# Kernel optimization log

Hardware: AMD Instinct MI355X
Metric: run time of the kernel (lower is better)

Reference implementation:

```python
import jax, jax.numpy as jnp
import numpy as np

B, S, E, H, U = 2048, 64, 512, 512, 512

def setup_inputs() -> dict:
    key = jax.random.key(0)
    ks = jax.random.split(key, 6)
    s = lambda d: 1.0 / np.sqrt(d)
    return {
        "features": jax.random.normal(ks[0], (B, S, E), jnp.float32),
        "hidden": jax.random.normal(ks[1], (B, H), jnp.float32),
        "W1": jax.random.normal(ks[2], (E, U), jnp.float32) * s(E),
        "b1": jnp.zeros((U,), jnp.float32),
        "W2": jax.random.normal(ks[3], (H, U), jnp.float32) * s(H),
        "b2": jnp.zeros((U,), jnp.float32),
        "Wv": jax.random.normal(ks[4], (U, 1), jnp.float32) * s(U),
        "bv": jnp.zeros((1,), jnp.float32),
    }

def reference(features, hidden, W1, b1, W2, b2, Wv, bv):
    # Bahdanau additive attention (dropout at inference = identity).
    h1 = jnp.einsum('bse,eu->bsu', features, W1) + b1          # [B,S,U]
    h2 = hidden @ W2 + b2                                       # [B,U]
    scores = jnp.tanh(h1 + h2[:, None, :]) @ Wv + bv            # [B,S,1]
    weights = jax.nn.softmax(scores, axis=1)                    # softmax over seq
    context = jnp.sum(weights * features, axis=1)               # [B,E]
    return context
```

## Files before the change

kernel.cpp:

```cpp
#include <hip/hip_runtime.h>

typedef _Float16 f16x8 __attribute__((ext_vector_type(8)));
typedef unsigned short u16x4 __attribute__((ext_vector_type(4)));
typedef float f32x4 __attribute__((ext_vector_type(4)));

#define VMWAIT(N) asm volatile("s_waitcnt vmcnt(" #N ")" ::: "memory")

__global__ void convert_w_kernel(const float* __restrict__ w1,
                                 const float* __restrict__ w2,
                                 unsigned short* __restrict__ w1img,
                                 unsigned short* __restrict__ w2img) {
    int u = blockIdx.x;
    int k = threadIdx.x + blockIdx.y * 256;
    size_t idx = (size_t)(k >> 5) * 16384 + (size_t)u * 32 + (k & 31);
    _Float16 h1 = (_Float16)w1[(size_t)k * 512 + u];
    _Float16 h2 = (_Float16)w2[(size_t)k * 512 + u];
    w1img[idx] = __builtin_bit_cast(unsigned short, h1);
    w2img[idx] = __builtin_bit_cast(unsigned short, h2);
}

__device__ __forceinline__ void stage_a64(const float* __restrict__ src,
                                          char* As, int tid) {
    const int row = tid >> 2, q = tid & 3;
    const float* p = src + (size_t)row * 512 + q * 4;
    const int sw2 = ((row >> 1) & 3) << 4;
    char* wb = As + row * 64;
    float4 va[4], vb[4];
#define AISS(V, G) { _Pragma("unroll") \
    for (int j_ = 0; j_ < 4; ++j_) V[j_] = *(const float4*)(p + ((G) * 4 + j_) * 16); }
#define APRC(V, G) { _Pragma("unroll") \
    for (int j_ = 0; j_ < 4; ++j_) { \
        const int i_ = (G) * 4 + j_; \
        u16x4 h_; \
        h_[0] = __builtin_bit_cast(unsigned short, (_Float16)V[j_].x); \
        h_[1] = __builtin_bit_cast(unsigned short, (_Float16)V[j_].y); \
        h_[2] = __builtin_bit_cast(unsigned short, (_Float16)V[j_].z); \
        h_[3] = __builtin_bit_cast(unsigned short, (_Float16)V[j_].w); \
        *(u16x4*)(wb + (i_ >> 1) * 4096 + ((q * 8 + (i_ & 1) * 32) ^ sw2)) = h_; } }
    AISS(va, 0); AISS(vb, 1);
    VMWAIT(4); APRC(va, 0); AISS(va, 2);
    VMWAIT(4); APRC(vb, 1); AISS(vb, 3);
    VMWAIT(4); APRC(va, 2); AISS(va, 4);
    VMWAIT(4); APRC(vb, 3); AISS(vb, 5);
    VMWAIT(4); APRC(va, 4); AISS(va, 6);
    VMWAIT(4); APRC(vb, 5); AISS(vb, 7);
    VMWAIT(4); APRC(va, 6);
    VMWAIT(0); APRC(vb, 7);
#undef AISS
#undef APRC
}

__device__ __forceinline__ void chunk_gemm(const char* __restrict__ bcol,
                                           const char* As, const int* aoff,
                                           f32x4 acc[4][4]) {
    f16x8 brA[4], brB[4], afA[4], afB[4];
    #pragma unroll
    for (int i = 0; i < 4; ++i)
        #pragma unroll
        for (int j = 0; j < 4; ++j) acc[i][j] = (f32x4){0.f, 0.f, 0.f, 0.f};
    #pragma unroll
    for (int j = 0; j < 4; ++j) brA[j] = *(const f16x8*)(bcol + j * 1024);
    #pragma unroll
    for (int j = 0; j < 4; ++j) brB[j] = *(const f16x8*)(bcol + 32768 + j * 1024);
    #pragma unroll
    for (int i = 0; i < 4; ++i) afA[i] = *(const f16x8*)(As + aoff[i]);

    #pragma unroll
    for (int tt = 0; tt < 8; ++tt) {
        const int t0 = 2 * tt, t1 = t0 + 1;
        if (t0 < 15) {
            #pragma unroll
            for (int i = 0; i < 4; ++i)
                afB[i] = *(const f16x8*)(As + t1 * 4096 + aoff[i]);
        }
        VMWAIT(4);
        #pragma unroll
        for (int i = 0; i < 4; ++i)
            #pragma unroll
            for (int j = 0; j < 4; ++j)
                acc[i][j] = __builtin_amdgcn_mfma_f32_16x16x32_f16(afA[i], brA[j], acc[i][j], 0, 0, 0);
        if (t0 < 14) {
            #pragma unroll
            for (int j = 0; j < 4; ++j)
                brA[j] = *(const f16x8*)(bcol + (t0 + 2) * 32768 + j * 1024);
        }
        if (t1 < 15) {
            #pragma unroll
            for (int i = 0; i < 4; ++i)
                afA[i] = *(const f16x8*)(As + (t1 + 1) * 4096 + aoff[i]);
        }
        if (t1 < 14) { VMWAIT(4); } else { VMWAIT(0); }
        #pragma unroll
        for (int i = 0; i < 4; ++i)
            #pragma unroll
            for (int j = 0; j < 4; ++j)
                acc[i][j] = __builtin_amdgcn_mfma_f32_16x16x32_f16(afB[i], brB[j], acc[i][j], 0, 0, 0);
        if (t1 < 14) {
            #pragma unroll
            for (int j = 0; j < 4; ++j)
                brB[j] = *(const f16x8*)(bcol + (t1 + 2) * 32768 + j * 1024);
        }
    }
}

__global__ __launch_bounds__(256, 2)
void h2_gemm_kernel(const float* __restrict__ hidden,
                    const char* __restrict__ w2img,
                    const float* __restrict__ b2,
                    float* __restrict__ h2o) {
    __shared__ char As[65536];
    const int tid = threadIdx.x, bm = blockIdx.x;
    const int lane = tid & 63, wid = tid >> 6;
    const int lane16 = lane & 15, g = lane >> 4;
    stage_a64(hidden + (size_t)bm * 32768, As, tid);
    __syncthreads();
    const int swA = (lane16 >> 1) & 3;
    int aoff[4];
    #pragma unroll
    for (int i = 0; i < 4; ++i)
        aoff[i] = (i * 16 + lane16) * 64 + ((g ^ swA) << 4);
    #pragma unroll
    for (int c = 0; c < 2; ++c) {
        const char* bcol = w2img + (size_t)(wid * 128 + c * 64 + lane16) * 64 + g * 16;
        f32x4 acc[4][4];
        chunk_gemm(bcol, As, aoff, acc);
        #pragma unroll
        for (int j = 0; j < 4; ++j) {
            int col = wid * 128 + c * 64 + j * 16 + lane16;
            float bb = b2[col];
            #pragma unroll
            for (int i = 0; i < 4; ++i)
                #pragma unroll
                for (int r = 0; r < 4; ++r)
                    h2o[(size_t)(bm * 64 + i * 16 + g * 4 + r) * 512 + col] = acc[i][j][r] + bb;
        }
    }
}

__global__ __launch_bounds__(256, 2)
void fused_all_kernel(const float* __restrict__ feat,
                      const char* __restrict__ w1img,
                      const float* __restrict__ h2,
                      const float* __restrict__ b1,
                      const float* __restrict__ wv,
                      float* __restrict__ out) {
    __shared__ char As[65536];
    __shared__ float spl[256];
    __shared__ float wsm[64];
    const int tid = threadIdx.x, bm = blockIdx.x;
    const int lane = tid & 63, wid = tid >> 6;
    const int lane16 = lane & 15, g = lane >> 4;

    stage_a64(feat + (size_t)bm * 32768, As, tid);
    __syncthreads();

    float hhv[8], wvv[8];
    #pragma unroll
    for (int j = 0; j < 8; ++j) {
        int u = wid * 128 + j * 16 + lane16;
        hhv[j] = b1[u] + h2[(size_t)bm * 512 + u];
        wvv[j] = wv[u];
    }
    VMWAIT(0);

    const int swA = (lane16 >> 1) & 3;
    int aoff[4];
    #pragma unroll
    for (int i = 0; i < 4; ++i)
        aoff[i] = (i * 16 + lane16) * 64 + ((g ^ swA) << 4);

    float sacc[16];
    #pragma unroll
    for (int x = 0; x < 16; ++x) sacc[x] = 0.f;

    #pragma unroll
    for (int c = 0; c < 2; ++c) {
        const char* bcol = w1img + (size_t)(wid * 128 + c * 64 + lane16) * 64 + g * 16;
        f32x4 acc[4][4];
        chunk_gemm(bcol, As, aoff, acc);
        #pragma unroll
        for (int i = 0; i < 4; ++i)
            #pragma unroll
            for (int r = 0; r < 4; ++r) {
                float s = 0.f;
                #pragma unroll
                for (int j = 0; j < 4; ++j) {
                    float h = acc[i][j][r] + hhv[c * 4 + j];
                    float ex = __expf(2.f * h);
                    s += (1.f - 2.f * __builtin_amdgcn_rcpf(ex + 1.f)) * wvv[c * 4 + j];
                }
                sacc[i * 4 + r] += s;
            }
    }

    #pragma unroll
    for (int i = 0; i < 4; ++i)
        #pragma unroll
        for (int r = 0; r < 4; ++r) {
            float s = sacc[i * 4 + r];
            s += __shfl_xor(s, 1); s += __shfl_xor(s, 2);
            s += __shfl_xor(s, 4); s += __shfl_xor(s, 8);
            if (lane16 == 0) spl[(i * 16 + g * 4 + r) * 4 + wid] = s;
        }
    __syncthreads();

    if (tid < 64) {
        float s = (spl[tid * 4 + 0] + spl[tid * 4 + 1]) +
                  (spl[tid * 4 + 2] + spl[tid * 4 + 3]);
        float m = s;
        #pragma unroll
        for (int off = 32; off; off >>= 1) m = fmaxf(m, __shfl_xor(m, off));
        float e = __expf(s - m);
        float sum = e;
        #pragma unroll
        for (int off = 32; off; off >>= 1) sum += __shfl_xor(sum, off);
        wsm[tid] = e / sum;
    }
    __syncthreads();

    {
        const int cseg = (tid >> 4) * 4096;
        const int cin = (tid & 15) * 4;
        float ax = 0.f, ay = 0.f;
        #pragma unroll 8
        for (int s = 0; s < 64; ++s) {
            unsigned v = *(const unsigned*)(As + cseg + s * 64 +
                                            (cin ^ (((s >> 1) & 3) << 4)));
            float w = wsm[s];
            ax += w * (float)__builtin_bit_cast(_Float16, (unsigned short)(v & 0xffffu));
            ay += w * (float)__builtin_bit_cast(_Float16, (unsigned short)(v >> 16));
        }
        ((float2*)out)[(size_t)bm * 256 + tid] = make_float2(ax, ay);
    }
}

extern "C" void kernel_launch(void* const* d_in, const int* in_sizes, int n_in,
                              void* d_out, int out_size, void* d_ws, size_t ws_size,
                              hipStream_t stream) {
    (void)in_sizes; (void)n_in; (void)out_size; (void)ws_size;
    const float* feat   = (const float*)d_in[0];
    const float* hidden = (const float*)d_in[1];
    const float* W1     = (const float*)d_in[2];
    const float* b1     = (const float*)d_in[3];
    const float* W2     = (const float*)d_in[4];
    const float* b2     = (const float*)d_in[5];
    const float* Wv     = (const float*)d_in[6];
    float* out = (float*)d_out;

    char* ws = (char*)d_ws;
    unsigned short* w1img = (unsigned short*)(ws);
    unsigned short* w2img = (unsigned short*)(ws + 524288);
    float* h2 = (float*)(ws + 1048576);

    convert_w_kernel<<<dim3(512, 2), dim3(256), 0, stream>>>(W1, W2, w1img, w2img);
    h2_gemm_kernel<<<dim3(32), dim3(256), 0, stream>>>(hidden, (const char*)w2img, b2, h2);
    fused_all_kernel<<<dim3(2048), dim3(256), 0, stream>>>(feat, (const char*)w1img, h2, b1, Wv, out);
}
```

Baseline: 149.6 us.

## Warp-specialize fused attention kernel with producer waves double-buffering feature tiles

The fused kernel now handles four batch rows per 512-thread block. Four consumer waves run the GEMM, tanh-score, softmax and context steps, while four producer waves load and convert the next batch's features into a second 64KB LDS buffer. Each consumer wave now covers 128 output columns in a single pass using 4x8 MFMA tiles, with s_setprio raised around the MFMA bursts. The aim is to hide the global feature loads behind MFMA work. In exchange, the block needs 128KB+ of LDS (which may limit it to one block per CU), carries higher register pressure, and adds raw barriers.

New measurement: 580.3 us. +288.0%, slower.

```diff
diff --git a/kernel.cpp b/kernel.cpp
--- a/kernel.cpp
+++ b/kernel.cpp
@@ -5,6 +5,18 @@
 typedef float f32x4 __attribute__((ext_vector_type(4)));
 
 #define VMWAIT(N) asm volatile("s_waitcnt vmcnt(" #N ")" ::: "memory")
+#define LGKM0()   asm volatile("s_waitcnt lgkmcnt(0)" ::: "memory")
+#define RBAR()    do { asm volatile("" ::: "memory"); __builtin_amdgcn_s_barrier(); \
+                       asm volatile("" ::: "memory"); } while (0)
+
+__device__ __forceinline__ u16x4 cvt4(float4 v) {
+    u16x4 h;
+    h[0] = __builtin_bit_cast(unsigned short, (_Float16)v.x);
+    h[1] = __builtin_bit_cast(unsigned short, (_Float16)v.y);
+    h[2] = __builtin_bit_cast(unsigned short, (_Float16)v.z);
+    h[3] = __builtin_bit_cast(unsigned short, (_Float16)v.w);
+    return h;
+}
 
 __global__ void convert_w_kernel(const float* __restrict__ w1,
                                  const float* __restrict__ w2,
@@ -31,12 +43,7 @@
 #define APRC(V, G) { _Pragma("unroll") \
     for (int j_ = 0; j_ < 4; ++j_) { \
         const int i_ = (G) * 4 + j_; \
-        u16x4 h_; \
-        h_[0] = __builtin_bit_cast(unsigned short, (_Float16)V[j_].x); \
-        h_[1] = __builtin_bit_cast(unsigned short, (_Float16)V[j_].y); \
-        h_[2] = __builtin_bit_cast(unsigned short, (_Float16)V[j_].z); \
-        h_[3] = __builtin_bit_cast(unsigned short, (_Float16)V[j_].w); \
-        *(u16x4*)(wb + (i_ >> 1) * 4096 + ((q * 8 + (i_ & 1) * 32) ^ sw2)) = h_; } }
+        *(u16x4*)(wb + (i_ >> 1) * 4096 + ((q * 8 + (i_ & 1) * 32) ^ sw2)) = cvt4(V[j_]); } }
     AISS(va, 0); AISS(vb, 1);
     VMWAIT(4); APRC(va, 0); AISS(va, 2);
     VMWAIT(4); APRC(vb, 1); AISS(vb, 3);
@@ -64,15 +71,12 @@
     for (int j = 0; j < 4; ++j) brB[j] = *(const f16x8*)(bcol + 32768 + j * 1024);
     #pragma unroll
     for (int i = 0; i < 4; ++i) afA[i] = *(const f16x8*)(As + aoff[i]);
-
     #pragma unroll
     for (int tt = 0; tt < 8; ++tt) {
         const int t0 = 2 * tt, t1 = t0 + 1;
-        if (t0 < 15) {
-            #pragma unroll
-            for (int i = 0; i < 4; ++i)
-                afB[i] = *(const f16x8*)(As + t1 * 4096 + aoff[i]);
-        }
+        #pragma unroll
+        for (int i = 0; i < 4; ++i)
+            afB[i] = *(const f16x8*)(As + t1 * 4096 + aoff[i]);
         VMWAIT(4);
         #pragma unroll
         for (int i = 0; i < 4; ++i)
@@ -114,11 +118,10 @@
     const int lane16 = lane & 15, g = lane >> 4;
     stage_a64(hidden + (size_t)bm * 32768, As, tid);
     __syncthreads();
-    const int swA = (lane16 >> 1) & 3;
     int aoff[4];
     #pragma unroll
     for (int i = 0; i < 4; ++i)
-        aoff[i] = (i * 16 + lane16) * 64 + ((g ^ swA) << 4);
+        aoff[i] = (i * 16 + lane16) * 64 + ((g ^ ((lane16 >> 1) & 3)) << 4);
     #pragma unroll
     for (int c = 0; c < 2; ++c) {
         const char* bcol = w2img + (size_t)(wid * 128 + c * 64 + lane16) * 64 + g * 16;
@@ -137,100 +140,190 @@
     }
 }
 
-__global__ __launch_bounds__(256, 2)
+__device__ __forceinline__ void chunk128(const char* __restrict__ bcol,
+                                         const char* As, const int* aoff,
+                                         f32x4 acc[4][8]) {
+    f16x8 brA[8], brB[8], afA[4], afB[4];
+    #pragma unroll
+    for (int i = 0; i < 4; ++i)
+        #pragma unroll
+        for (int j = 0; j < 8; ++j) acc[i][j] = (f32x4){0.f, 0.f, 0.f, 0.f};
+    #pragma unroll
+    for (int j = 0; j < 8; ++j) brA[j] = *(const f16x8*)(bcol + j * 1024);
+    #pragma unroll
+    for (int j = 0; j < 8; ++j) brB[j] = *(const f16x8*)(bcol + 32768 + j * 1024);
+    #pragma unroll
+    for (int i = 0; i < 4; ++i) afA[i] = *(const f16x8*)(As + aoff[i]);
+    #pragma unroll
+    for (int tt = 0; tt < 8; ++tt) {
+        const int t0 = 2 * tt, t1 = t0 + 1;
+        #pragma unroll
+        for (int i = 0; i < 4; ++i)
+            afB[i] = *(const f16x8*)(As + t1 * 4096 + aoff[i]);
+        VMWAIT(8);
+        __builtin_amdgcn_s_setprio(1);
+        #pragma unroll
+        for (int i = 0; i < 4; ++i)
+            #pragma unroll
+            for (int j = 0; j < 8; ++j)
+                acc[i][j] = __builtin_amdgcn_mfma_f32_16x16x32_f16(afA[i], brA[j], acc[i][j], 0, 0, 0);
+        __builtin_amdgcn_s_setprio(0);
+        if (t0 < 14) {
+            #pragma unroll
+            for (int j = 0; j < 8; ++j)
+                brA[j] = *(const f16x8*)(bcol + (t0 + 2) * 32768 + j * 1024);
+        }
+        if (t1 < 15) {
+            #pragma unroll
+            for (int i = 0; i < 4; ++i)
+                afA[i] = *(const f16x8*)(As + (t1 + 1) * 4096 + aoff[i]);
+        }
+        if (t1 < 14) { VMWAIT(8); } else { VMWAIT(0); }
+        __builtin_amdgcn_s_setprio(1);
+        #pragma unroll
+        for (int i = 0; i < 4; ++i)
+            #pragma unroll
+            for (int j = 0; j < 8; ++j)
+                acc[i][j] = __builtin_amdgcn_mfma_f32_16x16x32_f16(afB[i], brB[j], acc[i][j], 0, 0, 0);
+        __builtin_amdgcn_s_setprio(0);
+        if (t1 < 14) {
+            #pragma unroll
+            for (int j = 0; j < 8; ++j)
+                brB[j] = *(const f16x8*)(bcol + (t1 + 2) * 32768 + j * 1024);
+        }
+    }
+}
+
+__global__ __launch_bounds__(512, 2)
 void fused_all_kernel(const float* __restrict__ feat,
                       const char* __restrict__ w1img,
                       const float* __restrict__ h2,
                       const float* __restrict__ b1,
                       const float* __restrict__ wv,
                       float* __restrict__ out) {
-    __shared__ char As[65536];
+    __shared__ char As[2][65536];
     __shared__ float spl[256];
     __shared__ float wsm[64];
-    const int tid = threadIdx.x, bm = blockIdx.x;
-    const int lane = tid & 63, wid = tid >> 6;
-    const int lane16 = lane & 15, g = lane >> 4;
-
-    stage_a64(feat + (size_t)bm * 32768, As, tid);
-    __syncthreads();
-
-    float hhv[8], wvv[8];
-    #pragma unroll
-    for (int j = 0; j < 8; ++j) {
-        int u = wid * 128 + j * 16 + lane16;
-        hhv[j] = b1[u] + h2[(size_t)bm * 512 + u];
-        wvv[j] = wv[u];
-    }
-    VMWAIT(0);
-
-    const int swA = (lane16 >> 1) & 3;
+
+    const int tid = threadIdx.x;
+    const int b0 = blockIdx.x * 4;
+    const bool consumer = (tid < 256);
+    const int lane16 = tid & 15, g = (tid >> 4) & 3;
+    const int wid = tid >> 6;
+
+    {
+        const int row = tid >> 3, q = tid & 7;
+        const float* p = feat + (size_t)b0 * 32768 + (size_t)row * 512 + q * 4;
+        char* wb = As[0] + row * 64 + ((q * 8) ^ (((row >> 1) & 3) << 4));
+        float4 v[16];
+        #pragma unroll
+        for (int i = 0; i < 16; ++i) v[i] = *(const float4*)(p + i * 32);
+        VMWAIT(12);
+        #pragma unroll
+        for (int i = 0; i < 4; ++i)   *(u16x4*)(wb + i * 4096) = cvt4(v[i]);
+        VMWAIT(8);
+        #pragma unroll
+        for (int i = 4; i < 8; ++i)   *(u16x4*)(wb + i * 4096) = cvt4(v[i]);
+        VMWAIT(4);
+        #pragma unroll
+        for (int i = 8; i < 12; ++i)  *(u16x4*)(wb + i * 4096) = cvt4(v[i]);
+        VMWAIT(0);
+        #pragma unroll
+        for (int i = 12; i < 16; ++i) *(u16x4*)(wb + i * 4096) = cvt4(v[i]);
+    }
+    LGKM0();
+    RBAR();
+
     int aoff[4];
     #pragma unroll
     for (int i = 0; i < 4; ++i)
-        aoff[i] = (i * 16 + lane16) * 64 + ((g ^ swA) << 4);
-
-    float sacc[16];
-    #pragma unroll
-    for (int x = 0; x < 16; ++x) sacc[x] = 0.f;
-
-    #pragma unroll
-    for (int c = 0; c < 2; ++c) {
-        const char* bcol = w1img + (size_t)(wid * 128 + c * 64 + lane16) * 64 + g * 16;
-        f32x4 acc[4][4];
-        chunk_gemm(bcol, As, aoff, acc);
-        #pragma unroll
-        for (int i = 0; i < 4; ++i)
-            #pragma unroll
-            for (int r = 0; r < 4; ++r) {
-                float s = 0.f;
+        aoff[i] = (i * 16 + lane16) * 64 + ((g ^ ((lane16 >> 1) & 3)) << 4);
+    const char* bcol = w1img + (size_t)(wid * 128 + lane16) * 64 + g * 16;
+
+    const int prow = (tid & 255) >> 2, pq = tid & 3;
+    const int psw2 = ((prow >> 1) & 3) << 4;
+
+    #pragma unroll 1
+    for (int it = 0; it < 4; ++it) {
+        const int cur = it & 1;
+        const int b = b0 + it;
+        float4 pv[16];
+        if (consumer) {
+            f32x4 acc[4][8];
+            chunk128(bcol, As[cur], aoff, acc);
+            float hhv[8], wvv[8];
+            #pragma unroll
+            for (int j = 0; j < 8; ++j) {
+                int u = wid * 128 + j * 16 + lane16;
+                hhv[j] = b1[u] + h2[(size_t)b * 512 + u];
+                wvv[j] = wv[u];
+            }
+            #pragma unroll
+            for (int i = 0; i < 4; ++i) {
                 #pragma unroll
-                for (int j = 0; j < 4; ++j) {
-                    float h = acc[i][j][r] + hhv[c * 4 + j];
-                    float ex = __expf(2.f * h);
-                    s += (1.f - 2.f * __builtin_amdgcn_rcpf(ex + 1.f)) * wvv[c * 4 + j];
+                for (int r = 0; r < 4; ++r) {
+                    float s = 0.f;
+                    #pragma unroll
+                    for (int j = 0; j < 8; ++j) {
+                        float h = acc[i][j][r] + hhv[j];
+                        float ex = __expf(2.f * h);
+                        s += (1.f - 2.f * __builtin_amdgcn_rcpf(ex + 1.f)) * wvv[j];
+                    }
+                    s += __shfl_xor(s, 1); s += __shfl_xor(s, 2);
+                    s += __shfl_xor(s, 4); s += __shfl_xor(s, 8);
+                    if (lane16 == 0) spl[(i * 16 + g * 4 + r) * 4 + wid] = s;
                 }
-                sacc[i * 4 + r] += s;
             }
-    }
-
-    #pragma unroll
-    for (int i = 0; i < 4; ++i)
-        #pragma unroll
-        for (int r = 0; r < 4; ++r) {
-            float s = sacc[i * 4 + r];
-            s += __shfl_xor(s, 1); s += __shfl_xor(s, 2);
-            s += __shfl_xor(s, 4); s += __shfl_xor(s, 8);
-            if (lane16 == 0) spl[(i * 16 + g * 4 + r) * 4 + wid] = s;
-        }
-    __syncthreads();
-
-    if (tid < 64) {
-        float s = (spl[tid * 4 + 0] + spl[tid * 4 + 1]) +
-                  (spl[tid * 4 + 2] + spl[tid * 4 + 3]);
-        float m = s;
-        #pragma unroll
-        for (int off = 32; off; off >>= 1) m = fmaxf(m, __shfl_xor(m, off));
-        float e = __expf(s - m);
-        float sum = e;
-        #pragma unroll
-        for (int off = 32; off; off >>= 1) sum += __shfl_xor(sum, off);
-        wsm[tid] = e / sum;
-    }
-    __syncthreads();
-
-    {
-        const int cseg = (tid >> 4) * 4096;
-        const int cin = (tid & 15) * 4;
-        float ax = 0.f, ay = 0.f;
-        #pragma unroll 8
-        for (int s = 0; s < 64; ++s) {
-            unsigned v = *(const unsigned*)(As + cseg + s * 64 +
-                                            (cin ^ (((s >> 1) & 3) << 4)));
-            float w = wsm[s];
-            ax += w * (float)__builtin_bit_cast(_Float16, (unsigned short)(v & 0xffffu));
-            ay += w * (float)__builtin_bit_cast(_Float16, (unsigned short)(v >> 16));
-        }
-        ((float2*)out)[(size_t)bm * 256 + tid] = make_float2(ax, ay);
+            LGKM0();
+        } else if (it < 3) {
+            const float* p = feat + (size_t)(b + 1) * 32768 + (size_t)prow * 512 + pq * 4;
+            #pragma unroll
+            for (int i = 0; i < 16; ++i) pv[i] = *(const float4*)(p + i * 16);
+        }
+        RBAR();
+        if (tid < 64) {
+            float s = (spl[tid * 4 + 0] + spl[tid * 4 + 1]) +
+                      (spl[tid * 4 + 2] + spl[tid * 4 + 3]);
+            float m = s;
+            #pragma unroll
+            for (int off = 32; off; off >>= 1) m = fmaxf(m, __shfl_xor(m, off));
+            float e = __expf(s - m);
+            float sum = e;
+            #pragma unroll
+            for (int off = 32; off; off >>= 1) sum += __shfl_xor(sum, off);
+            wsm[tid] = e / sum;
+            LGKM0();
+        }
+        RBAR();
+        if (consumer) {
+            const int cseg = (tid >> 4) * 4096;
+            const int cin = (tid & 15) * 4;
+            float ax = 0.f, ay = 0.f;
+            #pragma unroll 8
+            for (int s = 0; s < 64; ++s) {
+                unsigned vv = *(const unsigned*)(As[cur] + cseg + s * 64 +
+                                                (cin ^ (((s >> 1) & 3) << 4)));
+                float w = wsm[s];
+                ax += w * (float)__builtin_bit_cast(_Float16, (unsigned short)(vv & 0xffffu));
+                ay += w * (float)__builtin_bit_cast(_Float16, (unsigned short)(vv >> 16));
+            }
+            ((float2*)out)[(size_t)b * 256 + tid] = make_float2(ax, ay);
+        } else if (it < 3) {
+            char* wb = As[cur ^ 1] + prow * 64;
+            VMWAIT(0);
+            #pragma unroll
+            for (int i = 0; i < 16; ++i)
+                *(u16x4*)(wb + (i >> 1) * 4096 + (((i & 1) * 32 + pq * 8) ^ psw2)) = cvt4(pv[i]);
+            const float* p = feat + (size_t)(b + 1) * 32768 + (size_t)prow * 512 + pq * 4 + 256;
+            #pragma unroll
+            for (int i = 0; i < 16; ++i) pv[i] = *(const float4*)(p + i * 16);
+            VMWAIT(0);
+            #pragma unroll
+            for (int i = 0; i < 16; ++i)
+                *(u16x4*)(wb + ((i + 16) >> 1) * 4096 + (((i & 1) * 32 + pq * 8) ^ psw2)) = cvt4(pv[i]);
+            LGKM0();
+        }
+        RBAR();
     }
 }
 
@@ -254,5 +347,5 @@
 
     convert_w_kernel<<<dim3(512, 2), dim3(256), 0, stream>>>(W1, W2, w1img, w2img);
     h2_gemm_kernel<<<dim3(32), dim3(256), 0, stream>>>(hidden, (const char*)w2img, b2, h2);
-    fused_all_kernel<<<dim3(2048), dim3(256), 0, stream>>>(feat, (const char*)w1img, h2, b1, Wv, out);
-}
+    fused_all_kernel<<<dim3(512), dim3(512), 0, stream>>>(feat, (const char*)w1img, h2, b1, Wv, out);
+}
```

## Make fused attention kernel persistent over four batches with prefetch of next features

Applied to the files above, without the earlier changes.

Each block of the fused kernel now handles four batch elements in sequence instead of one, and the grid shrinks to a quarter. While the MFMA GEMM for the current batch runs, the next batch's fp32 features are loaded into registers and converted to fp16. They are written into LDS after the context reduction, using a new swizzled layout. W1 fragments are double-buffered across the whole 32-step loop, and the h2/Wv bias terms are moved into shared memory. The aim is to hide global load latency behind MMA work, at the cost of much higher register pressure (a 32-entry pool) and fewer blocks to fill the CUs.

Measured after the change: 273.4 us. 82.8% more time.

```diff
diff --git a/kernel.cpp b/kernel.cpp
--- a/kernel.cpp
+++ b/kernel.cpp
@@ -5,6 +5,18 @@
 typedef float f32x4 __attribute__((ext_vector_type(4)));
 
 #define VMWAIT(N) asm volatile("s_waitcnt vmcnt(" #N ")" ::: "memory")
+#define LGKM0()   asm volatile("s_waitcnt lgkmcnt(0)" ::: "memory")
+#define FENCE()   asm volatile("" ::: "memory")
+#define RBAR()    do { FENCE(); __builtin_amdgcn_s_barrier(); FENCE(); } while (0)
+
+__device__ __forceinline__ u16x4 cvt4(float4 v) {
+    u16x4 h;
+    h[0] = __builtin_bit_cast(unsigned short, (_Float16)v.x);
+    h[1] = __builtin_bit_cast(unsigned short, (_Float16)v.y);
+    h[2] = __builtin_bit_cast(unsigned short, (_Float16)v.z);
+    h[3] = __builtin_bit_cast(unsigned short, (_Float16)v.w);
+    return h;
+}
 
 __global__ void convert_w_kernel(const float* __restrict__ w1,
                                  const float* __restrict__ w2,
@@ -31,12 +43,7 @@
 #define APRC(V, G) { _Pragma("unroll") \
     for (int j_ = 0; j_ < 4; ++j_) { \
         const int i_ = (G) * 4 + j_; \
-        u16x4 h_; \
-        h_[0] = __builtin_bit_cast(unsigned short, (_Float16)V[j_].x); \
-        h_[1] = __builtin_bit_cast(unsigned short, (_Float16)V[j_].y); \
-        h_[2] = __builtin_bit_cast(unsigned short, (_Float16)V[j_].z); \
-        h_[3] = __builtin_bit_cast(unsigned short, (_Float16)V[j_].w); \
-        *(u16x4*)(wb + (i_ >> 1) * 4096 + ((q * 8 + (i_ & 1) * 32) ^ sw2)) = h_; } }
+        *(u16x4*)(wb + (i_ >> 1) * 4096 + ((q * 8 + (i_ & 1) * 32) ^ sw2)) = cvt4(V[j_]); } }
     AISS(va, 0); AISS(vb, 1);
     VMWAIT(4); APRC(va, 0); AISS(va, 2);
     VMWAIT(4); APRC(vb, 1); AISS(vb, 3);
@@ -64,15 +71,12 @@
     for (int j = 0; j < 4; ++j) brB[j] = *(const f16x8*)(bcol + 32768 + j * 1024);
     #pragma unroll
     for (int i = 0; i < 4; ++i) afA[i] = *(const f16x8*)(As + aoff[i]);
-
     #pragma unroll
     for (int tt = 0; tt < 8; ++tt) {
         const int t0 = 2 * tt, t1 = t0 + 1;
-        if (t0 < 15) {
-            #pragma unroll
-            for (int i = 0; i < 4; ++i)
-                afB[i] = *(const f16x8*)(As + t1 * 4096 + aoff[i]);
-        }
+        #pragma unroll
+        for (int i = 0; i < 4; ++i)
+            afB[i] = *(const f16x8*)(As + t1 * 4096 + aoff[i]);
         VMWAIT(4);
         #pragma unroll
         for (int i = 0; i < 4; ++i)
@@ -114,11 +118,10 @@
     const int lane16 = lane & 15, g = lane >> 4;
     stage_a64(hidden + (size_t)bm * 32768, As, tid);
     __syncthreads();
-    const int swA = (lane16 >> 1) & 3;
     int aoff[4];
     #pragma unroll
     for (int i = 0; i < 4; ++i)
-        aoff[i] = (i * 16 + lane16) * 64 + ((g ^ swA) << 4);
+        aoff[i] = (i * 16 + lane16) * 64 + ((g ^ ((lane16 >> 1) & 3)) << 4);
     #pragma unroll
     for (int c = 0; c < 2; ++c) {
         const char* bcol = w2img + (size_t)(wid * 128 + c * 64 + lane16) * 64 + g * 16;
@@ -145,92 +148,196 @@
                       const float* __restrict__ wv,
                       float* __restrict__ out) {
     __shared__ char As[65536];
+    __shared__ float hhs[512];
+    __shared__ float wvs[512];
     __shared__ float spl[256];
     __shared__ float wsm[64];
-    const int tid = threadIdx.x, bm = blockIdx.x;
+
+    const int tid = threadIdx.x;
     const int lane = tid & 63, wid = tid >> 6;
     const int lane16 = lane & 15, g = lane >> 4;
-
-    stage_a64(feat + (size_t)bm * 32768, As, tid);
-    __syncthreads();
-
-    float hhv[8], wvv[8];
-    #pragma unroll
-    for (int j = 0; j < 8; ++j) {
-        int u = wid * 128 + j * 16 + lane16;
-        hhv[j] = b1[u] + h2[(size_t)bm * 512 + u];
-        wvv[j] = wv[u];
-    }
-    VMWAIT(0);
-
-    const int swA = (lane16 >> 1) & 3;
-    int aoff[4];
-    #pragma unroll
-    for (int i = 0; i < 4; ++i)
-        aoff[i] = (i * 16 + lane16) * 64 + ((g ^ swA) << 4);
-
-    float sacc[16];
-    #pragma unroll
-    for (int x = 0; x < 16; ++x) sacc[x] = 0.f;
-
-    #pragma unroll
-    for (int c = 0; c < 2; ++c) {
-        const char* bcol = w1img + (size_t)(wid * 128 + c * 64 + lane16) * 64 + g * 16;
+    const int b0 = blockIdx.x * 4;
+
+    {
+        float2 wv2 = *(const float2*)(wv + tid * 2);
+        float2 b12 = *(const float2*)(b1 + tid * 2);
+        float2 h22 = *(const float2*)(h2 + (size_t)b0 * 512 + tid * 2);
+        wvs[tid * 2] = wv2.x;  wvs[tid * 2 + 1] = wv2.y;
+        hhs[tid * 2] = b12.x + h22.x;  hhs[tid * 2 + 1] = b12.y + h22.y;
+    }
+    const char* aBase = (const char*)feat + (size_t)wid * 32768 + lane * 16;
+    {
+        const char* a0 = aBase + (size_t)b0 * 131072;
+        #pragma unroll
+        for (int gg = 0; gg < 4; ++gg) {
+            float4 v[8];
+            #pragma unroll
+            for (int p = 0; p < 8; ++p)
+                v[p] = *(const float4*)(a0 + (gg * 8 + p) * 1024);
+            #pragma unroll
+            for (int p = 0; p < 8; ++p) {
+                const int pi = gg * 8 + p;
+                const int row = wid * 16 + (pi >> 1);
+                const int t = (pi & 1) * 8 + (lane >> 3);
+                const int gq = (lane & 7) >> 1, inner = (lane & 1) * 8;
+                const int byte = t * 4096 + ((row ^ (t & 1)) * 64) +
+                                 (((gq ^ ((row >> 1) & 3)) << 4) + inner);
+                *(u16x4*)(As + byte) = cvt4(v[p]);
+            }
+        }
+    }
+    f16x8 brE[4], brO[4];
+    {
+        const char* bp0 = w1img + (size_t)(wid * 128 + lane16) * 64 + g * 16;
+        #pragma unroll
+        for (int j = 0; j < 4; ++j) brE[j] = *(const f16x8*)(bp0 + j * 1024);
+        FENCE();
+        #pragma unroll
+        for (int j = 0; j < 4; ++j) brO[j] = *(const f16x8*)(bp0 + 32768 + j * 1024);
+        FENCE();
+    }
+    LGKM0();
+    RBAR();
+
+    #pragma unroll 1
+    for (int it = 0; it < 4; ++it) {
+        const int bcur = b0 + it;
+        const int bnext = b0 + (it < 3 ? it + 1 : 3);
+        const char* aNext = aBase + (size_t)bnext * 131072;
+
+        u16x4 pool[32];
+        float4 win[3];
         f32x4 acc[4][4];
-        chunk_gemm(bcol, As, aoff, acc);
+        float sacc[16];
+        #pragma unroll
+        for (int x = 0; x < 16; ++x) sacc[x] = 0.f;
+        #pragma unroll
+        for (int i = 0; i < 4; ++i)
+            #pragma unroll
+            for (int j = 0; j < 4; ++j) acc[i][j] = (f32x4){0.f, 0.f, 0.f, 0.f};
+
+        #pragma unroll
+        for (int s = 0; s < 32; ++s) {
+            const int c = s >> 4, t = s & 15;
+            if (s >= 3) pool[s - 3] = cvt4(win[(s - 3) % 3]);
+            f16x8 af[4];
+            #pragma unroll
+            for (int i = 0; i < 4; ++i) {
+                const int row = i * 16 + lane16;
+                af[i] = *(const f16x8*)(As + t * 4096 + ((row ^ (t & 1)) * 64) +
+                                        ((g ^ ((row >> 1) & 3)) << 4));
+            }
+            const int sn = (s + 2) & 31;
+            const int cn = sn >> 4, tn = sn & 15;
+            const char* bpn = w1img + (size_t)tn * 32768 +
+                              (size_t)(wid * 128 + cn * 64 + lane16) * 64 + g * 16;
+            if ((s & 1) == 0) {
+                #pragma unroll
+                for (int i = 0; i < 4; ++i)
+                    #pragma unroll
+                    for (int j = 0; j < 4; ++j)
+                        acc[i][j] = __builtin_amdgcn_mfma_f32_16x16x32_f16(af[i], brE[j], acc[i][j], 0, 0, 0);
+                FENCE();
+                #pragma unroll
+                for (int j = 0; j < 4; ++j) brE[j] = *(const f16x8*)(bpn + j * 1024);
+            } else {
+                #pragma unroll
+                for (int i = 0; i < 4; ++i)
+                    #pragma unroll
+                    for (int j = 0; j < 4; ++j)
+                        acc[i][j] = __builtin_amdgcn_mfma_f32_16x16x32_f16(af[i], brO[j], acc[i][j], 0, 0, 0);
+                FENCE();
+                #pragma unroll
+                for (int j = 0; j < 4; ++j) brO[j] = *(const f16x8*)(bpn + j * 1024);
+            }
+            FENCE();
+            win[s % 3] = *(const float4*)(aNext + s * 1024);
+            FENCE();
+            if (t == 15) {
+                #pragma unroll
+                for (int i = 0; i < 4; ++i)
+                    #pragma unroll
+                    for (int r = 0; r < 4; ++r) {
+                        float sv = 0.f;
+                        #pragma unroll
+                        for (int j = 0; j < 4; ++j) {
+                            const int col = wid * 128 + c * 64 + j * 16 + lane16;
+                            float h = acc[i][j][r] + hhs[col];
+                            float ex = __expf(2.f * h);
+                            sv += (1.f - 2.f * __builtin_amdgcn_rcpf(ex + 1.f)) * wvs[col];
+                        }
+                        sacc[i * 4 + r] += sv;
+                    }
+                if (c == 0) {
+                    #pragma unroll
+                    for (int i = 0; i < 4; ++i)
+                        #pragma unroll
+                        for (int j = 0; j < 4; ++j) acc[i][j] = (f32x4){0.f, 0.f, 0.f, 0.f};
+                }
+            }
+        }
+        pool[29] = cvt4(win[29 % 3]);
+        pool[30] = cvt4(win[30 % 3]);
+        pool[31] = cvt4(win[31 % 3]);
+        float2 h22 = *(const float2*)(h2 + (size_t)bnext * 512 + tid * 2);
+        float2 b12 = *(const float2*)(b1 + tid * 2);
+        FENCE();
+
         #pragma unroll
         for (int i = 0; i < 4; ++i)
             #pragma unroll
             for (int r = 0; r < 4; ++r) {
-                float s = 0.f;
-                #pragma unroll
-                for (int j = 0; j < 4; ++j) {
-                    float h = acc[i][j][r] + hhv[c * 4 + j];
-                    float ex = __expf(2.f * h);
-                    s += (1.f - 2.f * __builtin_amdgcn_rcpf(ex + 1.f)) * wvv[c * 4 + j];
-                }
-                sacc[i * 4 + r] += s;
-            }
-    }
-
-    #pragma unroll
-    for (int i = 0; i < 4; ++i)
-        #pragma unroll
-        for (int r = 0; r < 4; ++r) {
-            float s = sacc[i * 4 + r];
-            s += __shfl_xor(s, 1); s += __shfl_xor(s, 2);
-            s += __shfl_xor(s, 4); s += __shfl_xor(s, 8);
-            if (lane16 == 0) spl[(i * 16 + g * 4 + r) * 4 + wid] = s;
-        }
-    __syncthreads();
-
-    if (tid < 64) {
-        float s = (spl[tid * 4 + 0] + spl[tid * 4 + 1]) +
-                  (spl[tid * 4 + 2] + spl[tid * 4 + 3]);
-        float m = s;
-        #pragma unroll
-        for (int off = 32; off; off >>= 1) m = fmaxf(m, __shfl_xor(m, off));
-        float e = __expf(s - m);
-        float sum = e;
-        #pragma unroll
-        for (int off = 32; off; off >>= 1) sum += __shfl_xor(sum, off);
-        wsm[tid] = e / sum;
-    }
-    __syncthreads();
-
-    {
-        const int cseg = (tid >> 4) * 4096;
-        const int cin = (tid & 15) * 4;
-        float ax = 0.f, ay = 0.f;
-        #pragma unroll 8
-        for (int s = 0; s < 64; ++s) {
-            unsigned v = *(const unsigned*)(As + cseg + s * 64 +
-                                            (cin ^ (((s >> 1) & 3) << 4)));
-            float w = wsm[s];
-            ax += w * (float)__builtin_bit_cast(_Float16, (unsigned short)(v & 0xffffu));
-            ay += w * (float)__builtin_bit_cast(_Float16, (unsigned short)(v >> 16));
-        }
-        ((float2*)out)[(size_t)bm * 256 + tid] = make_float2(ax, ay);
+                float s = sacc[i * 4 + r];
+                s += __shfl_xor(s, 1); s += __shfl_xor(s, 2);
+                s += __shfl_xor(s, 4); s += __shfl_xor(s, 8);
+                if (lane16 == 0) spl[(i * 16 + g * 4 + r) * 4 + wid] = s;
+            }
+        LGKM0();
+        RBAR();
+        if (tid < 64) {
+            float s = (spl[tid * 4 + 0] + spl[tid * 4 + 1]) +
+                      (spl[tid * 4 + 2] + spl[tid * 4 + 3]);
+            float m = s;
+            #pragma unroll
+            for (int off = 32; off; off >>= 1) m = fmaxf(m, __shfl_xor(m, off));
+            float e = __expf(s - m);
+            float sum = e;
+            #pragma unroll
+            for (int off = 32; off; off >>= 1) sum += __shfl_xor(sum, off);
+            wsm[tid] = e / sum;
+        }
+        LGKM0();
+        RBAR();
+        {
+            const int tpl = tid >> 4;
+            const int cin = (tid & 15) * 4;
+            float ax = 0.f, ay = 0.f;
+            #pragma unroll 8
+            for (int sr = 0; sr < 64; ++sr) {
+                const int byte = tpl * 4096 + ((sr ^ (tpl & 1)) * 64) +
+                                 ((((cin >> 4) ^ ((sr >> 1) & 3)) << 4) | (cin & 15));
+                unsigned vv = *(const unsigned*)(As + byte);
+                float w = wsm[sr];
+                ax += w * (float)__builtin_bit_cast(_Float16, (unsigned short)(vv & 0xffffu));
+                ay += w * (float)__builtin_bit_cast(_Float16, (unsigned short)(vv >> 16));
+            }
+            ((float2*)out)[(size_t)bcur * 256 + tid] = make_float2(ax, ay);
+        }
+        FENCE();
+        RBAR();
+        hhs[tid * 2]     = b12.x + h22.x;
+        hhs[tid * 2 + 1] = b12.y + h22.y;
+        #pragma unroll
+        for (int p = 0; p < 32; ++p) {
+            const int row = wid * 16 + (p >> 1);
+            const int t = (p & 1) * 8 + (lane >> 3);
+            const int gq = (lane & 7) >> 1, inner = (lane & 1) * 8;
+            const int byte = t * 4096 + ((row ^ (t & 1)) * 64) +
+                             (((gq ^ ((row >> 1) & 3)) << 4) + inner);
+            *(u16x4*)(As + byte) = pool[p];
+        }
+        LGKM0();
+        RBAR();
     }
 }
 
@@ -254,5 +361,5 @@
 
     convert_w_kernel<<<dim3(512, 2), dim3(256), 0, stream>>>(W1, W2, w1img, w2img);
     h2_gemm_kernel<<<dim3(32), dim3(256), 0, stream>>>(hidden, (const char*)w2img, b2, h2);
-    fused_all_kernel<<<dim3(2048), dim3(256), 0, stream>>>(feat, (const char*)w1img, h2, b1, Wv, out);
-}
+    fused_all_kernel<<<dim3(512), dim3(256), 0, stream>>>(feat, (const char*)w1img, h2, b1, Wv, out);
+}
```
